# Performance work log

Hardware: AMD Instinct MI355X
Metric: run time of the kernel (lower is better)

Reference implementation:

```python
import jax, jax.numpy as jnp
import numpy as np

EPS = 1e-6
B, CIN, COUT, N, S, M1, M2 = 4, 32, 32, 8192, 8, 12, 12
X, Y = 2 * M1 + 1, 2 * M2 + 1


def setup_inputs() -> dict:
    key = jax.random.key(0)
    ks = jax.random.split(key, 20)
    x = jax.random.normal(ks[0], (B, CIN, N), dtype=jnp.float32)
    loc = jax.random.uniform(ks[1], (B, N, 2), dtype=jnp.float32)
    # per-batch permutation of point indices; equal-size subdomains of N//S points
    ind = jnp.stack([jax.random.permutation(k, N) for k in jax.random.split(ks[2], B)]).astype(jnp.int32)
    ss = 1.0 / S
    sc = 1.0 / (CIN * COUT)
    u = lambda k, shp, s: s * jax.random.uniform(k, shp, dtype=jnp.float32)
    inp = {
        'x': x, 'loc': loc, 'ind': ind,
        'w1s_re': u(ks[3], (S, X, M2), ss), 'w1s_im': u(ks[4], (S, X, M2), ss),
        'w2s_re': u(ks[5], (S, M1 + 1, 1), ss), 'w2s_im': u(ks[6], (S, M1 + 1, 1), ss),
        'w1_re': u(ks[7], (CIN, COUT, X, M2), sc), 'w1_im': u(ks[8], (CIN, COUT, X, M2), sc),
        'w2_re': u(ks[9], (CIN, COUT, M1 + 1, 1), sc), 'w2_im': u(ks[10], (CIN, COUT, M1 + 1, 1), sc),
        'w1sb_re': u(ks[11], (S, X, M2), ss), 'w1sb_im': u(ks[12], (S, X, M2), ss),
        'w2sb_re': u(ks[13], (S, M1 + 1, 1), ss), 'w2sb_im': u(ks[14], (S, M1 + 1, 1), ss),
    }
    return inp


def _forward(x, loc, ind, w1s, w2s, w1, w2, w1sb, w2sb):
    b, cin, n = x.shape
    s, xg_dim, m2 = w1s.shape
    m1 = (xg_dim - 1) // 2
    xx, yy = 2 * m1 + 1, 2 * m2 + 1
    p = n // s
    norm = jnp.asarray(1.0 / np.sqrt(xx * yy), jnp.float32)

    # gather per-subdomain points (equal partitions replace the sep ragged split)
    xg = jnp.take_along_axis(x, ind[:, None, :], axis=2).reshape(b, cin, s, p)
    locg = jnp.take_along_axis(loc, ind[:, :, None], axis=1).reshape(b, s, p, 2)

    # per-subdomain min-max normalization of coords to [-pi, pi]
    om = jnp.swapaxes(locg, -1, -2)                      # [b,s,2,p]
    om = om - om.min(-1, keepdims=True)
    om = om / (om.max(-1, keepdims=True) + EPS)
    om = om * (2.0 * jnp.pi) - jnp.pi

    kx = (jnp.arange(xx) - m1).astype(jnp.float32)
    ky = (jnp.arange(yy) - m2).astype(jnp.float32)
    # exact (type-1) NUDFT basis; conj-wrapped adjoint = sum_p d_p exp(-i k.omega_p)
    E1 = jnp.exp(-1j * om[:, :, 0, :, None] * kx)        # [b,s,p,X]
    E2 = jnp.exp(-1j * om[:, :, 1, :, None] * ky)        # [b,s,p,Y]

    coef = jnp.einsum('bcsp,bspx,bspy->bcsxy', xg.astype(jnp.complex64), E1, E2) * norm

    i1 = coef[..., :m2]                                  # [b,c,s,X,m2]
    i2 = coef[:, :, :, :m1 + 1, m2:m2 + 1]               # [b,c,s,m1+1,1]

    i1 = jnp.einsum('bisxy,sxy->bixy', i1, w1s)
    i2 = jnp.einsum('bisxy,sxy->bixy', i2, w2s)
    i1 = jnp.einsum('bixy,ioxy->boxy', i1, w1)
    i2 = jnp.einsum('bixy,ioxy->boxy', i2, w2)
    i1 = jnp.einsum('boxy,sxy->bosxy', i1, w1sb)
    i2 = jnp.einsum('boxy,sxy->bosxy', i2, w2sb)

    cout = i1.shape[1]
    full = jnp.zeros((b, cout, s, xx, yy), jnp.complex64)
    full = full.at[..., :m2].set(i1)
    full = full.at[..., yy - m2:].set(jnp.conj(i1[..., ::-1, ::-1]))
    full = full.at[..., xx - m1 - 1:, m2:m2 + 1].set(jnp.conj(i2[..., ::-1, ::-1]))
    full = full.at[..., :m1 + 1, m2:m2 + 1].set(i2)      # overwrites center row (mode 0)

    # conj-wrapped forward NUFFT: sum_k c_k exp(+i k.omega_p)
    outc = jnp.einsum('bcsxy,bspx,bspy->bcsp', full, jnp.conj(E1), jnp.conj(E2)) * norm
    outr = outc.real                                     # [b,cout,s,p]

    # per-subdomain min-max renormalization back to input data range
    t = outr - outr.min(-1, keepdims=True)
    t = t / (t.max(-1, keepdims=True) + EPS)
    mn = xg.min(-1, keepdims=True)
    mx = xg.max(-1, keepdims=True)
    vals = t * (mx - mn) + mn                            # needs cin == cout

    # scatter back: output[b,:,ind[b,j]] = vals[b,:,j]
    inv = jnp.argsort(ind, axis=1)
    return jnp.take_along_axis(vals.reshape(b, cout, n), inv[:, None, :], axis=2)


def reference(x, loc, ind, w1s_re, w1s_im, w2s_re, w2s_im, w1_re, w1_im,
              w2_re, w2_im, w1sb_re, w1sb_im, w2sb_re, w2sb_im):
    c = lambda re, im: (re + 1j * im).astype(jnp.complex64)
    return _forward(x, loc, ind, c(w1s_re, w1s_im), c(w2s_re, w2s_im),
                    c(w1_re, w1_im), c(w2_re, w2_im),
                    c(w1sb_re, w1sb_im), c(w2sb_re, w2sb_im))
```

## Files before the change

kernel.cpp:

```cpp
#include <hip/hip_runtime.h>

#define B_ 4
#define C_ 32
#define N_ 8192
#define S_ 8
#define P_ 1024
#define NM_FWD 325
#define NM_INV 313
#define NORM_F 0.04f

#define PI_F 3.14159265358979f
#define TWOPI_F 6.28318530717959f

__device__ __forceinline__ unsigned pk_bf16(float a, float b){
  unsigned ab = __float_as_uint(a), bb = __float_as_uint(b);
  ab = (ab + 0x7FFFu + ((ab >> 16) & 1u)) >> 16;
  bb = (bb + 0x7FFFu + ((bb >> 16) & 1u)) & 0xFFFF0000u;
  return ab | bb;
}
#define UNPK_LO(u) __uint_as_float((u) << 16)
#define UNPK_HI(u) __uint_as_float((u) & 0xFFFF0000u)

__device__ __forceinline__ float blk_red(float v, float* red, bool is_min){
  int tid = threadIdx.x;
  red[tid] = v; __syncthreads();
  for (int off = blockDim.x >> 1; off > 0; off >>= 1){
    if (tid < off) red[tid] = is_min ? fminf(red[tid], red[tid+off]) : fmaxf(red[tid], red[tid+off]);
    __syncthreads();
  }
  float r = red[0]; __syncthreads();
  return r;
}

__global__ __launch_bounds__(256) void k_om(const float* __restrict__ loc,
                                            const int* __restrict__ ind,
                                            float* __restrict__ om){
  int b = blockIdx.x >> 3, s = blockIdx.x & 7;
  int tid = threadIdx.x;
  __shared__ float l0[P_], l1[P_];
  __shared__ float red[256];
  const int* indb = ind + b*N_ + s*P_;
  float mn0=1e30f, mx0=-1e30f, mn1=1e30f, mx1=-1e30f;
  for (int p = tid; p < P_; p += 256){
    int n = indb[p];
    float a = loc[(b*N_ + n)*2];
    float c = loc[(b*N_ + n)*2 + 1];
    l0[p] = a; l1[p] = c;
    mn0 = fminf(mn0, a); mx0 = fmaxf(mx0, a);
    mn1 = fminf(mn1, c); mx1 = fmaxf(mx1, c);
  }
  mn0 = blk_red(mn0, red, true);  mx0 = blk_red(mx0, red, false);
  mn1 = blk_red(mn1, red, true);  mx1 = blk_red(mx1, red, false);
  float i0 = TWOPI_F / (mx0 - mn0 + 1e-6f);
  float i1 = TWOPI_F / (mx1 - mn1 + 1e-6f);
  float* om0 = om + ((b*S_ + s)*2)*P_;
  float* om1 = om0 + P_;
  for (int p = tid; p < P_; p += 256){
    om0[p] = (l0[p] - mn0)*i0 - PI_F;
    om1[p] = (l1[p] - mn1)*i1 - PI_F;
  }
}

__global__ __launch_bounds__(512) void k_xg(const float* __restrict__ x,
                                            const int* __restrict__ ind,
                                            unsigned* __restrict__ xg_b,
                                            float* __restrict__ pmm){
  int blk = blockIdx.x;
  int part = blk & 3, bs = blk >> 2;
  int b = bs >> 3, s = bs & 7;
  int t = threadIdx.x;
  int c = t & 31, pl = t >> 5;
  __shared__ int inds[256];
  __shared__ float rmn[8*32], rmx[8*32];
  if (t < 256) inds[t] = ind[b*N_ + s*P_ + part*256 + t];
  __syncthreads();
  const float* xr = x + (b*C_ + c)*N_;
  float mn = 1e30f, mx = -1e30f;
  int pbase = part*256;
  #pragma unroll 4
  for (int k = 0; k < 16; ++k){
    int pp = pl + k*16;
    float v = xr[inds[pp]];
    float vp = __shfl_xor(v, 1);
    if ((c & 1) == 0)
      xg_b[(size_t)(bs*P_ + pbase + pp)*16 + (c >> 1)] = pk_bf16(v, vp);
    mn = fminf(mn, v); mx = fmaxf(mx, v);
  }
  mn = fminf(mn, __shfl_xor(mn, 32));
  mx = fmaxf(mx, __shfl_xor(mx, 32));
  int wid = t >> 6;
  if ((t & 63) < 32){ rmn[wid*32 + c] = mn; rmx[wid*32 + c] = mx; }
  __syncthreads();
  if (t < 32){
    float m0 = rmn[t], M0 = rmx[t];
    #pragma unroll
    for (int w = 1; w < 8; ++w){ m0 = fminf(m0, rmn[w*32+t]); M0 = fmaxf(M0, rmx[w*32+t]); }
    pmm[((bs*4 + part)*32 + t)*2]     = m0;
    pmm[((bs*4 + part)*32 + t)*2 + 1] = M0;
  }
}

__global__ __launch_bounds__(256) void k_wt(
    const float* __restrict__ w1s_re, const float* __restrict__ w1s_im,
    const float* __restrict__ w2s_re, const float* __restrict__ w2s_im,
    const float* __restrict__ w1_re,  const float* __restrict__ w1_im,
    const float* __restrict__ w2_re,  const float* __restrict__ w2_im,
    const float* __restrict__ w1sb_re,const float* __restrict__ w1sb_im,
    const float* __restrict__ w2sb_re,const float* __restrict__ w2sb_im,
    float* __restrict__ w1t, float* __restrict__ w1st, float* __restrict__ w1sbt){
  int q = blockIdx.x;
  int t = threadIdx.x;
  bool p1 = (q < 300);
  int x = p1 ? q % 25 : q - 300;
  int y = p1 ? q / 25 : 12;
  for (int idx = t; idx < 1024; idx += 256){
    float wre, wim;
    if (p1){ int wi = (idx*25 + x)*12 + y; wre = w1_re[wi]; wim = w1_im[wi]; }
    else   { int wi = idx*13 + x;          wre = w2_re[wi]; wim = w2_im[wi]; }
    w1t[(size_t)(q*1024 + idx)*2]     = wre;
    w1t[(size_t)(q*1024 + idx)*2 + 1] = wim;
  }
  if (t < 8){
    int s = t;
    float a, b2, c2, d2;
    if (p1){ int wi = (s*25+x)*12+y; a=w1s_re[wi]; b2=w1s_im[wi]; c2=w1sb_re[wi]; d2=w1sb_im[wi]; }
    else   { int wi = s*13+x;        a=w2s_re[wi]; b2=w2s_im[wi]; c2=w2sb_re[wi]; d2=w2sb_im[wi]; }
    w1st[(q*8+s)*2]   = a;  w1st[(q*8+s)*2+1]  = b2;
    w1sbt[(q*8+s)*2]  = c2; w1sbt[(q*8+s)*2+1] = d2;
  }
}

__global__ __launch_bounds__(64) void k_fwd(const float* __restrict__ om,
                                            const unsigned* __restrict__ xg_b,
                                            float* __restrict__ coef_part){
  int blk = blockIdx.x;
  int pp = blk & 7;
  int mc = (blk >> 3) % 6;
  int bs = blk / 48;
  int lane = threadIdx.x;
  int m = mc*64 + lane;
  int mcl = min(m, NM_FWD-1);
  int xo = mcl / 13, yo = mcl - xo*13;
  float kx = (float)(xo - 12), ky = (float)(yo - 12);
  int p0 = pp*128;
  __shared__ unsigned xs[128*16];
  __shared__ float2 oms[128];
  {
    const uint4* src = (const uint4*)(xg_b + (size_t)(bs*P_ + p0)*16);
    for (int i = lane; i < 512; i += 64) ((uint4*)xs)[i] = src[i];
    const float* o0p = om + bs*2*P_ + p0;
    const float* o1p = o0p + P_;
    for (int i = lane; i < 128; i += 64) oms[i] = make_float2(o0p[i], o1p[i]);
  }
  __syncthreads();
  float ar[32], ai[32];
  #pragma unroll
  for (int c = 0; c < 32; ++c){ ar[c] = 0.f; ai[c] = 0.f; }
  for (int p = 0; p < 128; ++p){
    float2 o = oms[p];
    float th = o.x*kx + o.y*ky;
    float sn, cs; __sincosf(th, &sn, &cs);
    const unsigned* xp = &xs[p*16];
    #pragma unroll
    for (int j4 = 0; j4 < 4; ++j4){
      uint4 g = *(const uint4*)&xp[j4*4];
      int cb = j4*8;
      float c0 = UNPK_LO(g.x), c1 = UNPK_HI(g.x);
      float c2 = UNPK_LO(g.y), c3 = UNPK_HI(g.y);
      float c4 = UNPK_LO(g.z), c5 = UNPK_HI(g.z);
      float c6 = UNPK_LO(g.w), c7 = UNPK_HI(g.w);
      ar[cb+0] += c0*cs; ai[cb+0] += c0*sn;
      ar[cb+1] += c1*cs; ai[cb+1] += c1*sn;
      ar[cb+2] += c2*cs; ai[cb+2] += c2*sn;
      ar[cb+3] += c3*cs; ai[cb+3] += c3*sn;
      ar[cb+4] += c4*cs; ai[cb+4] += c4*sn;
      ar[cb+5] += c5*cs; ai[cb+5] += c5*sn;
      ar[cb+6] += c6*cs; ai[cb+6] += c6*sn;
      ar[cb+7] += c7*cs; ai[cb+7] += c7*sn;
    }
  }
  if (m < NM_FWD){
    float* dst = coef_part + (size_t)((pp*32 + bs)*NM_FWD + m)*64;
    #pragma unroll
    for (int c = 0; c < 32; c += 2){
      *(float4*)&dst[c*2] = make_float4(ar[c]*NORM_F,   -ai[c]*NORM_F,
                                        ar[c+1]*NORM_F, -ai[c+1]*NORM_F);
    }
  }
}

__global__ __launch_bounds__(256) void k_mid(const float* __restrict__ coef_part,
    const float* __restrict__ w1t, const float* __restrict__ w1st,
    const float* __restrict__ w1sbt, unsigned* __restrict__ zpk){
  int blk = blockIdx.x;
  int b = blk / 79, qg = blk - b*79;
  int t = threadIdx.x;
  int w = t >> 6;
  int q = min(qg*4 + w, NM_INV-1);
  int lane = t & 63;
  int o = lane & 31;
  int hi = lane >> 5;
  bool p1 = (q < 300);
  int x = p1 ? q % 25 : q - 300;
  int y = p1 ? q / 25 : 12;
  int mf = x*13 + y;
  __shared__ float iv[4][64];
  float are = 0.f, aim = 0.f;
  #pragma unroll
  for (int ppl = 0; ppl < 4; ++ppl){
    int pp = hi*4 + ppl;
    #pragma unroll
    for (int s = 0; s < 8; ++s){
      const float* cp = coef_part + (size_t)((pp*32 + b*8 + s)*NM_FWD + mf)*64 + o*2;
      float cre = cp[0], cim = cp[1];
      float wre = w1st[(q*8+s)*2], wim = w1st[(q*8+s)*2+1];
      are += cre*wre - cim*wim;
      aim += cre*wim + cim*wre;
    }
  }
  are += __shfl_xor(are, 32);
  aim += __shfl_xor(aim, 32);
  if (hi == 0){ iv[w][o*2] = are; iv[w][o*2+1] = aim; }
  __syncthreads();
  float ore = 0.f, oim = 0.f;
  #pragma unroll
  for (int ii = 0; ii < 16; ++ii){
    int i = hi*16 + ii;
    float zre = iv[w][i*2], zim = iv[w][i*2+1];
    const float* wp = w1t + (size_t)(q*1024 + i*32 + o)*2;
    float wre = wp[0], wim = wp[1];
    ore += zre*wre - zim*wim;
    oim += zre*wim + zim*wre;
  }
  ore += __shfl_xor(ore, 32);
  oim += __shfl_xor(oim, 32);
  float scale = p1 ? 0.08f : ((x==12) ? 0.04f : 0.08f);
  #pragma unroll
  for (int si = 0; si < 4; ++si){
    int s = hi*4 + si;
    float wre = w1sbt[(q*8+s)*2], wim = w1sbt[(q*8+s)*2+1];
    float zre = (ore*wre - oim*wim)*scale;
    float zim = (ore*wim + oim*wre)*scale;
    zpk[(size_t)((b*8 + s)*NM_INV + q)*32 + o] = pk_bf16(zre, zim);
  }
}

__global__ __launch_bounds__(128) void k_inv(const float* __restrict__ om,
                                             const unsigned* __restrict__ zpk,
                                             float* __restrict__ routc){
  int blk = blockIdx.x;
  int pt = blk & 7;
  int oqp = (blk >> 3) & 1;
  int bs = blk >> 4;
  int t = threadIdx.x;
  int w = t >> 6, lane = t & 63;
  int oq = oqp*2 + w;
  int p0 = pt*128;
  __shared__ unsigned zs[64*32];
  float o0A = om[bs*2*P_ + p0 + lane];
  float o1A = om[bs*2*P_ + P_ + p0 + lane];
  float o0B = om[bs*2*P_ + p0 + lane + 64];
  float o1B = om[bs*2*P_ + P_ + p0 + lane + 64];
  float d0sA, d0cA; __sincosf(o0A, &d0sA, &d0cA);
  float d1sA, d1cA; __sincosf(o1A, &d1sA, &d1cA);
  float d0sB, d0cB; __sincosf(o0B, &d0sB, &d0cB);
  float d1sB, d1cB; __sincosf(o1B, &d1sB, &d1cB);
  float rsA, rcA; __sincosf(12.f*(o0A+o1A), &rsA, &rcA);
  float rsB, rcB; __sincosf(12.f*(o0B+o1B), &rsB, &rcB);
  float rreA = rcA, rimA = -rsA, rreB = rcB, rimB = -rsB;
  float freA = rreA, fimA = rimA, freB = rreB, fimB = rimB;
  int rowc = 0;
  float accA[8] = {0,0,0,0,0,0,0,0};
  float accB[8] = {0,0,0,0,0,0,0,0};
  const unsigned* zb = zpk + (size_t)bs*NM_INV*32;
  for (int chv = 0; chv < 5; ++chv){
    int m0 = chv*64;
    int mcount = min(64, NM_INV - m0);
    __syncthreads();
    for (int i = t*4; i < mcount*32; i += 512)
      *(uint4*)&zs[i] = *(const uint4*)&zb[m0*32 + i];
    __syncthreads();
    for (int m = 0; m < mcount; ++m){
      if (rowc == 25){
        float nrA = rreA*d1cA - rimA*d1sA, niA = rreA*d1sA + rimA*d1cA;
        rreA = nrA; rimA = niA; freA = rreA; fimA = rimA;
        float nrB = rreB*d1cB - rimB*d1sB, niB = rreB*d1sB + rimB*d1cB;
        rreB = nrB; rimB = niB; freB = rreB; fimB = rimB;
        rowc = 0;
      }
      uint4 ga = *(const uint4*)&zs[m*32 + oq*8];
      uint4 gb = *(const uint4*)&zs[m*32 + oq*8 + 4];
      float re0 = UNPK_LO(ga.x), im0 = UNPK_HI(ga.x);
      float re1 = UNPK_LO(ga.y), im1 = UNPK_HI(ga.y);
      float re2 = UNPK_LO(ga.z), im2 = UNPK_HI(ga.z);
      float re3 = UNPK_LO(ga.w), im3 = UNPK_HI(ga.w);
      float re4 = UNPK_LO(gb.x), im4 = UNPK_HI(gb.x);
      float re5 = UNPK_LO(gb.y), im5 = UNPK_HI(gb.y);
      float re6 = UNPK_LO(gb.z), im6 = UNPK_HI(gb.z);
      float re7 = UNPK_LO(gb.w), im7 = UNPK_HI(gb.w);
      accA[0] += re0*freA - im0*fimA;  accB[0] += re0*freB - im0*fimB;
      accA[1] += re1*freA - im1*fimA;  accB[1] += re1*freB - im1*fimB;
      accA[2] += re2*freA - im2*fimA;  accB[2] += re2*freB - im2*fimB;
      accA[3] += re3*freA - im3*fimA;  accB[3] += re3*freB - im3*fimB;
      accA[4] += re4*freA - im4*fimA;  accB[4] += re4*freB - im4*fimB;
      accA[5] += re5*freA - im5*fimA;  accB[5] += re5*freB - im5*fimB;
      accA[6] += re6*freA - im6*fimA;  accB[6] += re6*freB - im6*fimB;
      accA[7] += re7*freA - im7*fimA;  accB[7] += re7*freB - im7*fimB;
      float nfA = freA*d0cA - fimA*d0sA, niA = freA*d0sA + fimA*d0cA;
      freA = nfA; fimA = niA;
      float nfB = freB*d0cB - fimB*d0sB, niB = freB*d0sB + fimB*d0cB;
      freB = nfB; fimB = niB;
      ++rowc;
    }
  }
  float* outp = routc + (size_t)(bs*C_ + oq*8)*P_ + p0 + lane;
  #pragma unroll
  for (int j = 0; j < 8; ++j){
    outp[(size_t)j*P_]      = accA[j];
    outp[(size_t)j*P_ + 64] = accB[j];
  }
}

__global__ __launch_bounds__(256) void k_fin(const float* __restrict__ routc,
                                             const float* __restrict__ pmm,
                                             const int* __restrict__ ind,
                                             float* __restrict__ out){
  int blk = blockIdx.x;
  int o = blk & 31, s = (blk >> 5) & 7, b = blk >> 8;
  int bs = b*8 + s;
  int t = threadIdx.x;
  __shared__ float red[256];
  const float* rr = routc + (size_t)(bs*C_ + o)*P_;
  float v[4]; float mn = 1e30f, mx = -1e30f;
  #pragma unroll
  for (int k = 0; k < 4; ++k){
    v[k] = rr[t + k*256];
    mn = fminf(mn, v[k]); mx = fmaxf(mx, v[k]);
  }
  mn = blk_red(mn, red, true);
  mx = blk_red(mx, red, false);
  float xmn = 1e30f, xmx = -1e30f;
  #pragma unroll
  for (int part = 0; part < 4; ++part){
    xmn = fminf(xmn, pmm[((bs*4+part)*32 + o)*2]);
    xmx = fmaxf(xmx, pmm[((bs*4+part)*32 + o)*2 + 1]);
  }
  float scale = (xmx - xmn) / (mx - mn + 1e-6f);
  const int* indb = ind + b*N_ + s*P_;
  float* outb = out + (size_t)(b*C_ + o)*N_;
  #pragma unroll
  for (int k = 0; k < 4; ++k){
    int p = t + k*256;
    outb[indb[p]] = (v[k] - mn)*scale + xmn;
  }
}

extern "C" void kernel_launch(void* const* d_in, const int* in_sizes, int n_in,
                              void* d_out, int out_size, void* d_ws, size_t ws_size,
                              hipStream_t stream){
  const float* x      = (const float*)d_in[0];
  const float* loc    = (const float*)d_in[1];
  const int*   ind    = (const int*)  d_in[2];
  const float* w1s_re = (const float*)d_in[3];
  const float* w1s_im = (const float*)d_in[4];
  const float* w2s_re = (const float*)d_in[5];
  const float* w2s_im = (const float*)d_in[6];
  const float* w1_re  = (const float*)d_in[7];
  const float* w1_im  = (const float*)d_in[8];
  const float* w2_re  = (const float*)d_in[9];
  const float* w2_im  = (const float*)d_in[10];
  const float* w1sb_re= (const float*)d_in[11];
  const float* w1sb_im= (const float*)d_in[12];
  const float* w2sb_re= (const float*)d_in[13];
  const float* w2sb_im= (const float*)d_in[14];
  float* out = (float*)d_out;

  float* ws = (float*)d_ws;
  float*    om        = ws;
  unsigned* xg_b      = (unsigned*)(om + 65536);
  float*    pmm       = (float*)(xg_b + 524288);
  float*    coef_part = pmm + 8192;
  unsigned* zpk       = (unsigned*)(coef_part + 5324800);
  float*    w1t       = (float*)(zpk + 320512);
  float*    w1st      = w1t + 641024;
  float*    w1sbt     = w1st + 5008;
  float*    routc     = coef_part;

  k_om <<<32,   256, 0, stream>>>(loc, ind, om);
  k_xg <<<128,  512, 0, stream>>>(x, ind, xg_b, pmm);
  k_wt <<<NM_INV, 256, 0, stream>>>(w1s_re, w1s_im, w2s_re, w2s_im,
                                    w1_re, w1_im, w2_re, w2_im,
                                    w1sb_re, w1sb_im, w2sb_re, w2sb_im,
                                    w1t, w1st, w1sbt);
  k_fwd<<<1536, 64,  0, stream>>>(om, xg_b, coef_part);
  k_mid<<<316,  256, 0, stream>>>(coef_part, w1t, w1st, w1sbt, zpk);
  k_inv<<<512,  128, 0, stream>>>(om, zpk, routc);
  k_fin<<<1024, 256, 0, stream>>>(routc, pmm, ind, out);
}
```

Measured before the change: 232.8 us.

## Split inverse NUDFT over mode slabs with fp16 dot2 accumulation

The inverse kernel now splits the 313 modes into 4 slabs across blocks. Each block loads its whole slab into shared memory once, with no chunk loop, and processes 4 point groups per thread. It also switches the mode coefficients from bf16 to fp16 and uses packed fdot2 instructions for the complex multiply-accumulate. The final kernel sums the slab partials. The gather kernel is also split into twice as many blocks. This cuts ALU work and adds parallelism, at the cost of extra partial-sum memory traffic and reduced fp16 precision for the twiddles.

```diff
diff --git a/kernel.cpp b/kernel.cpp
--- a/kernel.cpp
+++ b/kernel.cpp
@@ -8,9 +8,14 @@
 #define NM_FWD 325
 #define NM_INV 313
 #define NORM_F 0.04f
+#define NSLAB 4
+#define SLABQ 79
+#define SLABSTRIDE 1048576
 
 #define PI_F 3.14159265358979f
 #define TWOPI_F 6.28318530717959f
+
+typedef __fp16 h2 __attribute__((ext_vector_type(2)));
 
 __device__ __forceinline__ unsigned pk_bf16(float a, float b){
   unsigned ab = __float_as_uint(a), bb = __float_as_uint(b);
@@ -66,19 +71,19 @@
                                             unsigned* __restrict__ xg_b,
                                             float* __restrict__ pmm){
   int blk = blockIdx.x;
-  int part = blk & 3, bs = blk >> 2;
+  int part = blk & 7, bs = blk >> 3;
   int b = bs >> 3, s = bs & 7;
   int t = threadIdx.x;
   int c = t & 31, pl = t >> 5;
-  __shared__ int inds[256];
+  __shared__ int inds[128];
   __shared__ float rmn[8*32], rmx[8*32];
-  if (t < 256) inds[t] = ind[b*N_ + s*P_ + part*256 + t];
+  if (t < 128) inds[t] = ind[b*N_ + s*P_ + part*128 + t];
   __syncthreads();
   const float* xr = x + (b*C_ + c)*N_;
   float mn = 1e30f, mx = -1e30f;
-  int pbase = part*256;
+  int pbase = part*128;
   #pragma unroll 4
-  for (int k = 0; k < 16; ++k){
+  for (int k = 0; k < 8; ++k){
     int pp = pl + k*16;
     float v = xr[inds[pp]];
     float vp = __shfl_xor(v, 1);
@@ -95,8 +100,8 @@
     float m0 = rmn[t], M0 = rmx[t];
     #pragma unroll
     for (int w = 1; w < 8; ++w){ m0 = fminf(m0, rmn[w*32+t]); M0 = fmaxf(M0, rmx[w*32+t]); }
-    pmm[((bs*4 + part)*32 + t)*2]     = m0;
-    pmm[((bs*4 + part)*32 + t)*2 + 1] = M0;
+    pmm[((bs*8 + part)*32 + t)*2]     = m0;
+    pmm[((bs*8 + part)*32 + t)*2 + 1] = M0;
   }
 }
 
@@ -241,87 +246,97 @@
     float wre = w1sbt[(q*8+s)*2], wim = w1sbt[(q*8+s)*2+1];
     float zre = (ore*wre - oim*wim)*scale;
     float zim = (ore*wim + oim*wre)*scale;
-    zpk[(size_t)((b*8 + s)*NM_INV + q)*32 + o] = pk_bf16(zre, zim);
-  }
-}
-
-__global__ __launch_bounds__(128) void k_inv(const float* __restrict__ om,
+    h2 zh = __builtin_amdgcn_cvt_pkrtz(zre, zim);
+    zpk[(size_t)((b*8 + s)*NM_INV + q)*32 + o] = __builtin_bit_cast(unsigned, zh);
+  }
+}
+
+__global__ __launch_bounds__(256) void k_inv(const float* __restrict__ om,
                                              const unsigned* __restrict__ zpk,
-                                             float* __restrict__ routc){
+                                             float* __restrict__ routp){
   int blk = blockIdx.x;
-  int pt = blk & 7;
-  int oqp = (blk >> 3) & 1;
+  int slab = blk & 3;
+  int pt = (blk >> 2) & 3;
   int bs = blk >> 4;
   int t = threadIdx.x;
-  int w = t >> 6, lane = t & 63;
-  int oq = oqp*2 + w;
-  int p0 = pt*128;
-  __shared__ unsigned zs[64*32];
-  float o0A = om[bs*2*P_ + p0 + lane];
-  float o1A = om[bs*2*P_ + P_ + p0 + lane];
-  float o0B = om[bs*2*P_ + p0 + lane + 64];
-  float o1B = om[bs*2*P_ + P_ + p0 + lane + 64];
-  float d0sA, d0cA; __sincosf(o0A, &d0sA, &d0cA);
-  float d1sA, d1cA; __sincosf(o1A, &d1sA, &d1cA);
-  float d0sB, d0cB; __sincosf(o0B, &d0sB, &d0cB);
-  float d1sB, d1cB; __sincosf(o1B, &d1sB, &d1cB);
-  float rsA, rcA; __sincosf(12.f*(o0A+o1A), &rsA, &rcA);
-  float rsB, rcB; __sincosf(12.f*(o0B+o1B), &rsB, &rcB);
-  float rreA = rcA, rimA = -rsA, rreB = rcB, rimB = -rsB;
-  float freA = rreA, fimA = rimA, freB = rreB, fimB = rimB;
-  int rowc = 0;
-  float accA[8] = {0,0,0,0,0,0,0,0};
-  float accB[8] = {0,0,0,0,0,0,0,0};
-  const unsigned* zb = zpk + (size_t)bs*NM_INV*32;
-  for (int chv = 0; chv < 5; ++chv){
-    int m0 = chv*64;
-    int mcount = min(64, NM_INV - m0);
-    __syncthreads();
-    for (int i = t*4; i < mcount*32; i += 512)
-      *(uint4*)&zs[i] = *(const uint4*)&zb[m0*32 + i];
-    __syncthreads();
-    for (int m = 0; m < mcount; ++m){
-      if (rowc == 25){
-        float nrA = rreA*d1cA - rimA*d1sA, niA = rreA*d1sA + rimA*d1cA;
-        rreA = nrA; rimA = niA; freA = rreA; fimA = rimA;
-        float nrB = rreB*d1cB - rimB*d1sB, niB = rreB*d1sB + rimB*d1cB;
-        rreB = nrB; rimB = niB; freB = rreB; fimB = rimB;
-        rowc = 0;
+  int oq = t >> 6, lane = t & 63;
+  int p0 = pt*256;
+  int q0 = slab*SLABQ;
+  int cnt = min(SLABQ, NM_INV - q0);
+  __shared__ unsigned zs[SLABQ*32];
+  {
+    const uint4* src = (const uint4*)(zpk + (size_t)bs*NM_INV*32 + q0*32);
+    int n4 = cnt*8;
+    for (int i = t; i < n4; i += 256) ((uint4*)zs)[i] = src[i];
+  }
+  int y0 = q0 / 25, x0 = q0 - y0*25;
+  float kx0 = (float)(x0 - 12), ky0 = (float)(y0 - 12);
+  float d0c[4], d0s[4], d1c[4], d1s[4];
+  float fre[4], fim[4], rre[4], rim[4];
+  #pragma unroll
+  for (int k = 0; k < 4; ++k){
+    float o0 = om[bs*2*P_ + p0 + lane + k*64];
+    float o1 = om[bs*2*P_ + P_ + p0 + lane + k*64];
+    __sincosf(o0, &d0s[k], &d0c[k]);
+    __sincosf(o1, &d1s[k], &d1c[k]);
+    float thf = kx0*o0 + ky0*o1;
+    float sf, cf; __sincosf(thf, &sf, &cf);
+    fre[k] = cf; fim[k] = sf;
+    float thr = -12.f*o0 + ky0*o1;
+    float sr, cr; __sincosf(thr, &sr, &cr);
+    rre[k] = cr; rim[k] = sr;
+  }
+  float acc[4][8];
+  #pragma unroll
+  for (int k = 0; k < 4; ++k)
+    #pragma unroll
+    for (int j = 0; j < 8; ++j) acc[k][j] = 0.f;
+  int rowc = x0;
+  __syncthreads();
+  for (int m = 0; m < cnt; ++m){
+    if (rowc == 25){
+      #pragma unroll
+      for (int k = 0; k < 4; ++k){
+        float nr = rre[k]*d1c[k] - rim[k]*d1s[k];
+        float ni = rre[k]*d1s[k] + rim[k]*d1c[k];
+        rre[k] = nr; rim[k] = ni;
+        fre[k] = nr; fim[k] = ni;
       }
-      uint4 ga = *(const uint4*)&zs[m*32 + oq*8];
-      uint4 gb = *(const uint4*)&zs[m*32 + oq*8 + 4];
-      float re0 = UNPK_LO(ga.x), im0 = UNPK_HI(ga.x);
-      float re1 = UNPK_LO(ga.y), im1 = UNPK_HI(ga.y);
-      float re2 = UNPK_LO(ga.z), im2 = UNPK_HI(ga.z);
-      float re3 = UNPK_LO(ga.w), im3 = UNPK_HI(ga.w);
-      float re4 = UNPK_LO(gb.x), im4 = UNPK_HI(gb.x);
-      float re5 = UNPK_LO(gb.y), im5 = UNPK_HI(gb.y);
-      float re6 = UNPK_LO(gb.z), im6 = UNPK_HI(gb.z);
-      float re7 = UNPK_LO(gb.w), im7 = UNPK_HI(gb.w);
-      accA[0] += re0*freA - im0*fimA;  accB[0] += re0*freB - im0*fimB;
-      accA[1] += re1*freA - im1*fimA;  accB[1] += re1*freB - im1*fimB;
-      accA[2] += re2*freA - im2*fimA;  accB[2] += re2*freB - im2*fimB;
-      accA[3] += re3*freA - im3*fimA;  accB[3] += re3*freB - im3*fimB;
-      accA[4] += re4*freA - im4*fimA;  accB[4] += re4*freB - im4*fimB;
-      accA[5] += re5*freA - im5*fimA;  accB[5] += re5*freB - im5*fimB;
-      accA[6] += re6*freA - im6*fimA;  accB[6] += re6*freB - im6*fimB;
-      accA[7] += re7*freA - im7*fimA;  accB[7] += re7*freB - im7*fimB;
-      float nfA = freA*d0cA - fimA*d0sA, niA = freA*d0sA + fimA*d0cA;
-      freA = nfA; fimA = niA;
-      float nfB = freB*d0cB - fimB*d0sB, niB = freB*d0sB + fimB*d0cB;
-      freB = nfB; fimB = niB;
-      ++rowc;
+      rowc = 0;
     }
-  }
-  float* outp = routc + (size_t)(bs*C_ + oq*8)*P_ + p0 + lane;
-  #pragma unroll
-  for (int j = 0; j < 8; ++j){
-    outp[(size_t)j*P_]      = accA[j];
-    outp[(size_t)j*P_ + 64] = accB[j];
-  }
-}
-
-__global__ __launch_bounds__(256) void k_fin(const float* __restrict__ routc,
+    const unsigned* zrow = &zs[m*32 + oq*8];
+    uint4 ga = *(const uint4*)zrow;
+    uint4 gb = *(const uint4*)(zrow + 4);
+    h2 z0 = __builtin_bit_cast(h2, ga.x), z1 = __builtin_bit_cast(h2, ga.y);
+    h2 z2 = __builtin_bit_cast(h2, ga.z), z3 = __builtin_bit_cast(h2, ga.w);
+    h2 z4 = __builtin_bit_cast(h2, gb.x), z5 = __builtin_bit_cast(h2, gb.y);
+    h2 z6 = __builtin_bit_cast(h2, gb.z), z7 = __builtin_bit_cast(h2, gb.w);
+    #pragma unroll
+    for (int k = 0; k < 4; ++k){
+      h2 fp = __builtin_amdgcn_cvt_pkrtz(fre[k], -fim[k]);
+      acc[k][0] = __builtin_amdgcn_fdot2(z0, fp, acc[k][0], false);
+      acc[k][1] = __builtin_amdgcn_fdot2(z1, fp, acc[k][1], false);
+      acc[k][2] = __builtin_amdgcn_fdot2(z2, fp, acc[k][2], false);
+      acc[k][3] = __builtin_amdgcn_fdot2(z3, fp, acc[k][3], false);
+      acc[k][4] = __builtin_amdgcn_fdot2(z4, fp, acc[k][4], false);
+      acc[k][5] = __builtin_amdgcn_fdot2(z5, fp, acc[k][5], false);
+      acc[k][6] = __builtin_amdgcn_fdot2(z6, fp, acc[k][6], false);
+      acc[k][7] = __builtin_amdgcn_fdot2(z7, fp, acc[k][7], false);
+      float nf = fre[k]*d0c[k] - fim[k]*d0s[k];
+      float ni = fre[k]*d0s[k] + fim[k]*d0c[k];
+      fre[k] = nf; fim[k] = ni;
+    }
+    ++rowc;
+  }
+  float* outp = routp + (size_t)slab*SLABSTRIDE + (size_t)(bs*C_ + oq*8)*P_ + p0 + lane;
+  #pragma unroll
+  for (int j = 0; j < 8; ++j)
+    #pragma unroll
+    for (int k = 0; k < 4; ++k)
+      outp[(size_t)j*P_ + k*64] = acc[k][j];
+}
+
+__global__ __launch_bounds__(256) void k_fin(const float* __restrict__ routp,
                                              const float* __restrict__ pmm,
                                              const int* __restrict__ ind,
                                              float* __restrict__ out){
@@ -330,20 +345,25 @@
   int bs = b*8 + s;
   int t = threadIdx.x;
   __shared__ float red[256];
-  const float* rr = routc + (size_t)(bs*C_ + o)*P_;
+  const float* rr = routp + (size_t)(bs*C_ + o)*P_;
   float v[4]; float mn = 1e30f, mx = -1e30f;
   #pragma unroll
   for (int k = 0; k < 4; ++k){
-    v[k] = rr[t + k*256];
-    mn = fminf(mn, v[k]); mx = fmaxf(mx, v[k]);
+    int p = t + k*256;
+    float acc = rr[p];
+    #pragma unroll
+    for (int sl = 1; sl < NSLAB; ++sl)
+      acc += rr[(size_t)sl*SLABSTRIDE + p];
+    v[k] = acc;
+    mn = fminf(mn, acc); mx = fmaxf(mx, acc);
   }
   mn = blk_red(mn, red, true);
   mx = blk_red(mx, red, false);
   float xmn = 1e30f, xmx = -1e30f;
   #pragma unroll
-  for (int part = 0; part < 4; ++part){
-    xmn = fminf(xmn, pmm[((bs*4+part)*32 + o)*2]);
-    xmx = fmaxf(xmx, pmm[((bs*4+part)*32 + o)*2 + 1]);
+  for (int part = 0; part < 8; ++part){
+    xmn = fminf(xmn, pmm[((bs*8+part)*32 + o)*2]);
+    xmx = fmaxf(xmx, pmm[((bs*8+part)*32 + o)*2 + 1]);
   }
   float scale = (xmx - xmn) / (mx - mn + 1e-6f);
   const int* indb = ind + b*N_ + s*P_;
@@ -379,21 +399,21 @@
   float*    om        = ws;
   unsigned* xg_b      = (unsigned*)(om + 65536);
   float*    pmm       = (float*)(xg_b + 524288);
-  float*    coef_part = pmm + 8192;
+  float*    coef_part = pmm + 16384;
   unsigned* zpk       = (unsigned*)(coef_part + 5324800);
   float*    w1t       = (float*)(zpk + 320512);
   float*    w1st      = w1t + 641024;
   float*    w1sbt     = w1st + 5008;
-  float*    routc     = coef_part;
+  float*    routp     = coef_part;
 
   k_om <<<32,   256, 0, stream>>>(loc, ind, om);
-  k_xg <<<128,  512, 0, stream>>>(x, ind, xg_b, pmm);
+  k_xg <<<256,  512, 0, stream>>>(x, ind, xg_b, pmm);
   k_wt <<<NM_INV, 256, 0, stream>>>(w1s_re, w1s_im, w2s_re, w2s_im,
                                     w1_re, w1_im, w2_re, w2_im,
                                     w1sb_re, w1sb_im, w2sb_re, w2sb_im,
                                     w1t, w1st, w1sbt);
   k_fwd<<<1536, 64,  0, stream>>>(om, xg_b, coef_part);
   k_mid<<<316,  256, 0, stream>>>(coef_part, w1t, w1st, w1sbt, zpk);
-  k_inv<<<512,  128, 0, stream>>>(om, zpk, routc);
-  k_fin<<<1024, 256, 0, stream>>>(routc, pmm, ind, out);
-}
+  k_inv<<<512,  256, 0, stream>>>(om, zpk, routp);
+  k_fin<<<1024, 256, 0, stream>>>(routp, pmm, ind, out);
+}
```

Result: faster. 186.6 us (-19.8%).
